# Performance work log

Hardware: AMD Instinct MI355X
Metric: run time of the kernel (lower is better)

Reference implementation:

```python
import jax, jax.numpy as jnp
import numpy as np


def setup_inputs() -> dict:
    V, D, E = 4096, 128, 12288
    key = jax.random.key(0)
    k1, k2, k3 = jax.random.split(key, 3)
    features = jax.random.normal(k1, (V, D), dtype=jnp.float32)
    # random self-loop-free edge list
    v0 = jax.random.randint(k2, (E,), 0, V)
    off = jax.random.randint(k3, (E,), 1, V)
    v1 = (v0 + off) % V
    edges = jnp.stack([v0, v1]).astype(jnp.int32)  # [2, E]
    # manifold-style neighbor matrix: interior edges share 2 faces
    neighbor = (jnp.zeros((V, V), jnp.int32)
                .at[edges[0], edges[1]].set(2)
                .at[edges[1], edges[0]].set(2))
    return {"features": features, "edges": edges, "neighbor": neighbor}


def _collapse(features, edges, neighbor):
    """Greedy heap-order edge collapse. The heap is built once and only popped,
    so pop order == edges sorted by priority ||f[v0]||^2 + ||f[v1]||^2.
    Returns merge matrix A (f_out = A @ f_in), alive vertex mask, final count."""
    V = neighbor.shape[0]
    target = jnp.int32(V // 2)
    pri = jnp.sum(features * features, axis=1)          # [V]
    epri = pri[edges[0]] + pri[edges[1]]                # [E]
    order = jnp.argsort(epri)                           # heappop order (stable ties)
    alive0 = jnp.ones((V,), bool)
    A0 = jnp.eye(V, dtype=jnp.float32)
    cnt0 = jnp.int32(V)

    def step(carry, e):
        alive, n, A, cnt = carry
        v0 = edges[0, e]
        v1 = edges[1, e]
        do = (cnt > target) & alive[v0] & alive[v1] & (n[v0, v1] == 2)
        # merged neighbor row for v0; v1 dies
        r = (n[v0] + n[v1]).at[v0].set(0).at[v1].set(0)
        row0 = jnp.where(do, r, n[v0])
        row1 = jnp.where(do, jnp.zeros_like(r), n[v1])
        n = (n.at[v0, :].set(row0).at[:, v0].set(row0)
              .at[v1, :].set(row1).at[:, v1].set(row1))
        arow = jnp.where(do, 0.5 * (A[v0] + A[v1]), A[v0])
        A = A.at[v0].set(arow)
        alive = alive.at[v1].set(alive[v1] & jnp.logical_not(do))
        cnt = cnt - do.astype(jnp.int32)
        return (alive, n, A, cnt), None

    (alive, n, A, cnt), _ = jax.lax.scan(step, (alive0, neighbor, A0, cnt0), order)
    return A, alive, cnt


def reference(features, edges, neighbor):
    edges = edges.astype(jnp.int32)
    A, alive, cnt = _collapse(features, edges, neighbor)
    # clean_up() compacts removed vertices; under jit we mask dead rows instead
    pooled = (A @ features) * alive[:, None].astype(features.dtype)
    return pooled, alive, cnt
```

## Files before the change

### kernel.cpp

```cpp
#include <hip/hip_runtime.h>
#include <stdint.h>

#define V 4096
#define D 128
#define E 12288
#define NPAD 16384
#define HALF 8192
#define TARGET 2048
#define MAXM (V - TARGET)
#define ROWU32 256
#define CAP 16
#define SCANCAP 24

#define WAIT_VM0   0x0F70
#define WAIT_LGKM0 0xC07F

#define WS_N      0u
#define WS_PRI    (V * ROWU32 * 4u)
#define WS_KEYS   (WS_PRI + V * 4u)
#define WS_PK     (WS_KEYS + NPAD * 8u)
#define WS_PAIRS  (WS_PK + E * 4u)
#define WS_MCOUNT (WS_PAIRS + MAXM * 4u)
#define WS_ALIVE  (WS_MCOUNT + 16u)

typedef const __attribute__((address_space(1))) unsigned* gas1_t;
typedef __attribute__((address_space(3))) unsigned* las3_t;

__device__ __forceinline__ unsigned getf(const uint4& r, int c) {
    unsigned lo = (c & 2) ? r.z : r.x;
    unsigned hi = (c & 2) ? r.w : r.y;
    return (c & 1) ? hi : lo;
}
__device__ __forceinline__ void orf(uint4& r, int c, unsigned bits) {
    if (c == 0) r.x |= bits; else if (c == 1) r.y |= bits;
    else if (c == 2) r.z |= bits; else r.w |= bits;
}
__device__ __forceinline__ void andf(uint4& r, int c, unsigned msk) {
    if (c == 0) r.x &= msk; else if (c == 1) r.y &= msk;
    else if (c == 2) r.z &= msk; else r.w &= msk;
}

__global__ void k_scatter(const int* __restrict__ edges, unsigned* __restrict__ n32) {
    int e = blockIdx.x * 256 + threadIdx.x;
    if (e < E) {
        int a = edges[e], b = edges[E + e];
        atomicOr(&n32[a * ROWU32 + (b >> 4)], 2u << ((b & 15) * 2));
        atomicOr(&n32[b * ROWU32 + (a >> 4)], 2u << ((a & 15) * 2));
    }
}

__global__ void k_pri(const float* __restrict__ f, float* __restrict__ pri) {
    int v = blockIdx.x * 256 + threadIdx.x;
    if (v < V) {
        const float* p = f + v * D;
        float r[8];
#pragma unroll
        for (int j = 0; j < 8; j++) r[j] = __fmul_rn(p[j], p[j]);
        for (int i = 8; i < D; i += 8) {
#pragma unroll
            for (int j = 0; j < 8; j++)
                r[j] = __fadd_rn(r[j], __fmul_rn(p[i + j], p[i + j]));
        }
        float s01 = __fadd_rn(r[0], r[1]);
        float s23 = __fadd_rn(r[2], r[3]);
        float s45 = __fadd_rn(r[4], r[5]);
        float s67 = __fadd_rn(r[6], r[7]);
        pri[v] = __fadd_rn(__fadd_rn(s01, s23), __fadd_rn(s45, s67));
    }
}

__global__ void k_keys(const int* __restrict__ edges, const float* __restrict__ pri,
                       unsigned long long* __restrict__ keys) {
    int s = blockIdx.x * 256 + threadIdx.x;
    if (s < NPAD) {
        unsigned long long rec;
        if (s < E) {
            int a = edges[s], b = edges[E + s];
            float k = __fadd_rn(pri[a], pri[b]);
            rec = ((unsigned long long)__float_as_uint(k) << 32) | (unsigned)s;
        } else {
            rec = (0xFFFFFFFFull << 32) | (unsigned)s;
        }
        keys[s] = rec;
    }
}

__launch_bounds__(1024)
__global__ void k_sort2(unsigned long long* __restrict__ keys) {
    __shared__ unsigned long long srt[HALF];
    const int tid = threadIdx.x;
    unsigned long long* base = keys + blockIdx.x * HALF;
    for (int s = tid; s < HALF; s += 1024) srt[s] = base[s];
    __syncthreads();
    for (int k = 2; k <= HALF; k <<= 1) {
        for (int j = k >> 1; j >= 1; j >>= 1) {
            for (int i = tid; i < HALF; i += 1024) {
                int ixj = i ^ j;
                if (ixj > i) {
                    unsigned long long x = srt[i], y = srt[ixj];
                    bool up = ((i & k) == 0);
                    if ((x > y) == up) { srt[i] = y; srt[ixj] = x; }
                }
            }
            __syncthreads();
        }
    }
    for (int s = tid; s < HALF; s += 1024) base[s] = srt[s];
}

__launch_bounds__(64)
__global__ void k_mergepath(const unsigned long long* __restrict__ keys,
                            const int* __restrict__ edges, unsigned* __restrict__ pkG) {
    int t = blockIdx.x * 64 + threadIdx.x;
    if (t >= E / 64) return;
    const unsigned long long* A = keys;
    const unsigned long long* B = keys + HALF;
    int d = t * 64;
    int lo = d > HALF ? d - HALF : 0;
    int hi = d < HALF ? d : HALF;
    while (lo < hi) {
        int mid = (lo + hi) >> 1;
        if (A[mid] < B[d - 1 - mid]) lo = mid + 1; else hi = mid;
    }
    int ia = lo, ib = d - lo;
    for (int o = d; o < d + 64; o++) {
        bool takeA = (ib >= HALF) || (ia < HALF && A[ia] < B[ib]);
        unsigned long long r = takeA ? A[ia++] : B[ib++];
        int e = (int)(r & 0xFFFFFFFFull);
        int a = edges[e], b = edges[E + e];
        pkG[o] = ((unsigned)a << 16) | (unsigned)b;
    }
}

__launch_bounds__(64, 1)
__global__ void k_collapse(const unsigned* __restrict__ pkG, unsigned* n32,
                           unsigned* __restrict__ pairsG, int* __restrict__ mcountG,
                           uint8_t* __restrict__ aliveG, float* __restrict__ out) {
    __shared__ unsigned shRows[2 * CAP * ROWU32];
    __shared__ uint8_t alive[V];
    const int lane = threadIdx.x;
    for (int v = lane; v < V; v += 64) alive[v] = 1;
    __builtin_amdgcn_s_waitcnt(WAIT_LGKM0);

    int cnt = V, mcount = 0;
    bool done = false;

    for (int w = 0; w < E && !done; w += 64) {
        __builtin_amdgcn_s_waitcnt(WAIT_VM0);
        unsigned pkv = pkG[w + lane];
        const int a = (int)(pkv >> 16), b = (int)(pkv & 0xFFFFu);
        unsigned wv = *(volatile unsigned*)(n32 + a * ROWU32 + (b >> 4));
        unsigned fv = (wv >> ((b & 15) * 2)) & 3u;
        bool dec = !(alive[a] && alive[b]);

        while (!done) {
            if (!dec && fv != 2u) dec = true;
            unsigned long long mF = __ballot(!dec);
            if (!mF) break;
            int limit = cnt - TARGET; if (limit > CAP) limit = CAP;

            unsigned long long accLanes = 0ull;
            unsigned long long B0 = 0ull, B1 = 0ull;
            int nacc = 0, scanned = 0;
            {
                unsigned long long mIt = mF;
                while (mIt && nacc < limit && scanned < SCANCAP) {
                    int i = __ffsll(mIt) - 1; mIt &= mIt - 1ull;
                    int ai = __shfl(a, i), bi = __shfl(b, i);
                    unsigned ha = ((unsigned)ai * 2654435761u) >> 25;
                    unsigned hb = ((unsigned)bi * 2654435761u) >> 25;
                    unsigned long long m0 = 0ull, m1 = 0ull;
                    if (ha & 64) m1 |= 1ull << (ha & 63); else m0 |= 1ull << (ha & 63);
                    if (hb & 64) m1 |= 1ull << (hb & 63); else m0 |= 1ull << (hb & 63);
                    bool conf = ((B0 & m0) | (B1 & m1)) != 0ull;
                    if (!conf) { accLanes |= 1ull << i; nacc++; }
                    B0 |= m0; B1 |= m1;
                    scanned++;
                }
            }

            __builtin_amdgcn_s_waitcnt(WAIT_VM0);
            {
                unsigned long long am = accLanes; int k = 0;
                while (am) {
                    int i = __ffsll(am) - 1; am &= am - 1ull;
                    int v0 = __shfl(a, i), v1 = __shfl(b, i);
                    __builtin_amdgcn_global_load_lds(
                        (gas1_t)(n32 + v0 * ROWU32 + lane * 4),
                        (las3_t)(shRows + (2 * k) * ROWU32), 16, 0, 0);
                    __builtin_amdgcn_global_load_lds(
                        (gas1_t)(n32 + v1 * ROWU32 + lane * 4),
                        (las3_t)(shRows + (2 * k + 1) * ROWU32), 16, 0, 0);
                    k++;
                }
            }
            __builtin_amdgcn_s_waitcnt(WAIT_VM0);
            __builtin_amdgcn_s_waitcnt(WAIT_LGKM0);

            unsigned long long keptLanes = 0ull;
            {
                uint4 RBU = make_uint4(0u, 0u, 0u, 0u);
                uint4 MV0 = make_uint4(0u, 0u, 0u, 0u);
                unsigned long long am = accLanes; int k = 0;
                while (am) {
                    int i = __ffsll(am) - 1; am &= am - 1ull;
                    int v0 = __shfl(a, i), v1 = __shfl(b, i);
                    uint4 rb = *((const uint4*)(shRows + (2 * k + 1) * ROWU32) + lane);
                    bool c = false;
                    if ((v0 >> 6) == lane)
                        c |= ((getf(RBU, (v0 >> 4) & 3) >> ((v0 & 15) * 2)) & 3u) != 0u;
                    if ((v1 >> 6) == lane)
                        c |= ((getf(RBU, (v1 >> 4) & 3) >> ((v1 & 15) * 2)) & 3u) != 0u;
                    c |= ((rb.x & MV0.x) | (rb.y & MV0.y) |
                          (rb.z & MV0.z) | (rb.w & MV0.w)) != 0u;
                    if (__ballot(c) == 0ull) {
                        keptLanes |= 1ull << i;
                        RBU.x |= rb.x; RBU.y |= rb.y; RBU.z |= rb.z; RBU.w |= rb.w;
                        if ((v0 >> 6) == lane) orf(MV0, (v0 >> 4) & 3, 3u << ((v0 & 15) * 2));
                    }
                    k++;
                }
            }

            {
                unsigned long long am = accLanes; int k = 0;
                while (am) {
                    int i = __ffsll(am) - 1; am &= am - 1ull;
                    if ((keptLanes >> i) & 1ull) {
                        int v0 = __shfl(a, i), v1 = __shfl(b, i);
                        uint4 ra = *((const uint4*)(shRows + (2 * k) * ROWU32) + lane);
                        uint4 rb = *((const uint4*)(shRows + (2 * k + 1) * ROWU32) + lane);
                        uint4 rr;
                        rr.x = ra.x | rb.x | ((ra.x & rb.x & 0xAAAAAAAAu) >> 1);
                        rr.y = ra.y | rb.y | ((ra.y & rb.y & 0xAAAAAAAAu) >> 1);
                        rr.z = ra.z | rb.z | ((ra.z & rb.z & 0xAAAAAAAAu) >> 1);
                        rr.w = ra.w | rb.w | ((ra.w & rb.w & 0xAAAAAAAAu) >> 1);
                        if ((v0 >> 6) == lane) andf(rr, (v0 >> 4) & 3, ~(3u << ((v0 & 15) * 2)));
                        if ((v1 >> 6) == lane) andf(rr, (v1 >> 4) & 3, ~(3u << ((v1 & 15) * 2)));
                        *((uint4*)(n32 + v0 * ROWU32) + lane) = rr;
                        *((uint4*)(shRows + (2 * k) * ROWU32) + lane) = rr;
                        int sh0 = (v0 & 15) * 2, wi0 = v0 >> 4;
#pragma unroll
                        for (int c = 0; c < 4; c++) {
                            unsigned bb = getf(rb, c);
                            if (!bb) continue;
                            unsigned aa = getf(ra, c), vvv = getf(rr, c);
                            int xbase = (lane << 6) + (c << 4);
                            unsigned t = bb;
                            while (t) {
                                int q = (__ffs(t) - 1) >> 1;
                                t &= ~(3u << (q * 2));
                                int x = xbase + q;
                                if (x != v0 && x != v1) {
                                    unsigned dx =
                                        (((aa >> (q * 2)) ^ (vvv >> (q * 2))) & 3u) << sh0;
                                    if (dx) atomicXor(n32 + x * ROWU32 + wi0, dx);
                                }
                            }
                        }
                        if (lane == 0) {
                            alive[v1] = 0;
                            pairsG[mcount] = ((unsigned)v0 << 16) | (unsigned)v1;
                        }
                        mcount++; cnt--;
                    }
                    k++;
                }
            }
            __builtin_amdgcn_s_waitcnt(WAIT_LGKM0);

            {
                int slot = -1, fld = 0;
                unsigned long long am = accLanes; int k = 0;
                while (am) {
                    int i = __ffsll(am) - 1; am &= am - 1ull;
                    if ((keptLanes >> i) & 1ull) {
                        int v0 = __shfl(a, i), v1 = __shfl(b, i);
                        if (a == v1 || b == v1) dec = true;
                        if (lane == i) dec = true;
                        if (b == v0) { slot = 2 * k; fld = a; }
                        else if (a == v0) { slot = 2 * k; fld = b; }
                    }
                    k++;
                }
                if (slot >= 0 && !dec)
                    fv = (shRows[slot * ROWU32 + (fld >> 4)] >> ((fld & 15) * 2)) & 3u;
            }
            if (cnt == TARGET) done = true;
        }
    }

    for (int v = lane; v < V; v += 64) {
        uint8_t ao = alive[v];
        aliveG[v] = ao;
        out[V * D + v] = ao ? 1.0f : 0.0f;
    }
    if (lane == 0) { mcountG[0] = mcount; out[V * D + V] = (float)cnt; }
}

__launch_bounds__(256)
__global__ void k_apply(const float* __restrict__ f, const unsigned* __restrict__ pairsG,
                        const int* __restrict__ mcountG, float* __restrict__ out) {
    __shared__ unsigned pl[MAXM];
    __shared__ int rootL[256];
    __shared__ float wL[256];
    const int tid = threadIdx.x;
    const int mc = mcountG[0];
    for (int j = tid; j < mc; j += 256) pl[j] = pairsG[j];
    __syncthreads();
    int cur = blockIdx.x * 256 + tid;
    float w = 1.0f;
    for (int j = 0; j < mc; j++) {
        unsigned p = pl[j];
        int v0 = (int)(p >> 16), v1 = (int)(p & 0xFFFFu);
        if (cur == v1) { cur = v0; w *= 0.5f; }
        else if (cur == v0) w *= 0.5f;
    }
    rootL[tid] = cur;
    wL[tid] = w;
    __syncthreads();
    const int sub = tid >> 7;
    const int d = tid & 127;
    for (int s = 0; s < 256; s += 2) {
        int idx = s + sub;
        int vv = blockIdx.x * 256 + idx;
        atomicAdd(&out[rootL[idx] * D + d], wL[idx] * f[vv * D + d]);
    }
}

extern "C" void kernel_launch(void* const* d_in, const int* in_sizes, int n_in,
                              void* d_out, int out_size, void* d_ws, size_t ws_size,
                              hipStream_t stream) {
    (void)in_sizes; (void)n_in; (void)out_size; (void)ws_size;
    const float* features = (const float*)d_in[0];
    const int* edges = (const int*)d_in[1];
    uint8_t* ws = (uint8_t*)d_ws;
    unsigned* n32 = (unsigned*)(ws + WS_N);
    float* pri = (float*)(ws + WS_PRI);
    unsigned long long* keys = (unsigned long long*)(ws + WS_KEYS);
    unsigned* pkG = (unsigned*)(ws + WS_PK);
    unsigned* pairsG = (unsigned*)(ws + WS_PAIRS);
    int* mcountG = (int*)(ws + WS_MCOUNT);
    uint8_t* aliveG = ws + WS_ALIVE;
    float* out = (float*)d_out;

    hipMemsetAsync(n32, 0, (size_t)V * ROWU32 * 4, stream);
    hipMemsetAsync(out, 0, (size_t)V * D * sizeof(float), stream);
    k_pri<<<(V + 255) / 256, 256, 0, stream>>>(features, pri);
    k_scatter<<<(E + 255) / 256, 256, 0, stream>>>(edges, n32);
    k_keys<<<(NPAD + 255) / 256, 256, 0, stream>>>(edges, pri, keys);
    k_sort2<<<2, 1024, 0, stream>>>(keys);
    k_mergepath<<<(E / 64 + 63) / 64, 64, 0, stream>>>(keys, edges, pkG);
    k_collapse<<<1, 64, 0, stream>>>(pkG, n32, pairsG, mcountG, aliveG, out);
    k_apply<<<V / 256, 256, 0, stream>>>(features, pairsG, mcountG, out);
}
```

Before: 3.826 ms.

## Parallelize collapse batch conflict check and row merges across lane groups

```diff
diff --git a/kernel.cpp b/kernel.cpp
--- a/kernel.cpp
+++ b/kernel.cpp
@@ -10,7 +10,6 @@
 #define MAXM (V - TARGET)
 #define ROWU32 256
 #define CAP 16
-#define SCANCAP 24
 
 #define WAIT_VM0   0x0F70
 #define WAIT_LGKM0 0xC07F
@@ -30,10 +29,6 @@
     unsigned lo = (c & 2) ? r.z : r.x;
     unsigned hi = (c & 2) ? r.w : r.y;
     return (c & 1) ? hi : lo;
-}
-__device__ __forceinline__ void orf(uint4& r, int c, unsigned bits) {
-    if (c == 0) r.x |= bits; else if (c == 1) r.y |= bits;
-    else if (c == 2) r.z |= bits; else r.w |= bits;
 }
 __device__ __forceinline__ void andf(uint4& r, int c, unsigned msk) {
     if (c == 0) r.x &= msk; else if (c == 1) r.y &= msk;
@@ -137,10 +132,13 @@
                            unsigned* __restrict__ pairsG, int* __restrict__ mcountG,
                            uint8_t* __restrict__ aliveG, float* __restrict__ out) {
     __shared__ unsigned shRows[2 * CAP * ROWU32];
-    __shared__ uint8_t alive[V];
+    __shared__ uint8_t  alive[V];
+    __shared__ uint8_t  shV2S[V];
+    __shared__ unsigned shCand[CAP];
+    __shared__ unsigned shConf[CAP];
     const int lane = threadIdx.x;
-    for (int v = lane; v < V; v += 64) alive[v] = 1;
-    __builtin_amdgcn_s_waitcnt(WAIT_LGKM0);
+    for (int v = lane; v < V; v += 64) { alive[v] = 1; shV2S[v] = 0xFF; }
+    __syncthreads();
 
     int cnt = V, mcount = 0;
     bool done = false;
@@ -158,134 +156,125 @@
             unsigned long long mF = __ballot(!dec);
             if (!mF) break;
             int limit = cnt - TARGET; if (limit > CAP) limit = CAP;
-
-            unsigned long long accLanes = 0ull;
-            unsigned long long B0 = 0ull, B1 = 0ull;
-            int nacc = 0, scanned = 0;
+            int flagged = (int)__popcll(mF);
+            int nacc = flagged < limit ? flagged : limit;
+
+            int myK = -1;
+            if (!dec) {
+                int rank = (int)__popcll(mF & ((1ull << lane) - 1ull));
+                if (rank < limit) { myK = rank; shCand[rank] = pkv; }
+            }
+            if (lane < CAP) shConf[lane] = 0u;
+            __syncthreads();
+
+            __builtin_amdgcn_s_waitcnt(WAIT_VM0);
+            for (int k = 0; k < nacc; k++) {
+                unsigned cp = shCand[k];
+                int v0 = (int)(cp >> 16), v1 = (int)(cp & 0xFFFFu);
+                __builtin_amdgcn_global_load_lds(
+                    (gas1_t)(n32 + v0 * ROWU32 + lane * 4),
+                    (las3_t)(shRows + (2 * k) * ROWU32), 16, 0, 0);
+                __builtin_amdgcn_global_load_lds(
+                    (gas1_t)(n32 + v1 * ROWU32 + lane * 4),
+                    (las3_t)(shRows + (2 * k + 1) * ROWU32), 16, 0, 0);
+            }
+            __builtin_amdgcn_s_waitcnt(WAIT_VM0);
+            __syncthreads();
+
+            for (int pp = lane; pp < CAP * CAP; pp += 64) {
+                int k = pp >> 4, j = pp & 15;
+                if (j < k && k < nacc) {
+                    unsigned cj = shCand[j], ck = shCand[k];
+                    int v0j = (int)(cj >> 16), v1j = (int)(cj & 0xFFFFu);
+                    int v0k = (int)(ck >> 16), v1k = (int)(ck & 0xFFFFu);
+                    bool c = (v0k == v0j) || (v0k == v1j) || (v1k == v0j) || (v1k == v1j);
+                    c |= ((shRows[(2*j+1)*ROWU32 + (v0k >> 4)] >> ((v0k & 15)*2)) & 3u) != 0u;
+                    c |= ((shRows[(2*j+1)*ROWU32 + (v1k >> 4)] >> ((v1k & 15)*2)) & 3u) != 0u;
+                    c |= ((shRows[(2*k+1)*ROWU32 + (v0j >> 4)] >> ((v0j & 15)*2)) & 3u) != 0u;
+                    if (c) atomicOr(&shConf[k], 1u << j);
+                }
+            }
+            __syncthreads();
+
+            unsigned kept = 0u;
+            for (int k = 0; k < nacc; k++)
+                if (shConf[k] == 0u) kept |= 1u << k;
+            int nk = __popc(kept);
+            if (myK >= 0 && ((kept >> myK) & 1u)) dec = true;
+
+            if (lane < nacc && ((kept >> lane) & 1u)) {
+                unsigned cp = shCand[lane];
+                int v0 = (int)(cp >> 16), v1 = (int)(cp & 0xFFFFu);
+                alive[v1] = 0;
+                shV2S[v0] = (uint8_t)(2 * lane);
+                int r = __popc(kept & ((1u << lane) - 1u));
+                pairsG[mcount + r] = cp;
+            }
+            mcount += nk; cnt -= nk;
+            __syncthreads();
+
             {
-                unsigned long long mIt = mF;
-                while (mIt && nacc < limit && scanned < SCANCAP) {
-                    int i = __ffsll(mIt) - 1; mIt &= mIt - 1ull;
-                    int ai = __shfl(a, i), bi = __shfl(b, i);
-                    unsigned ha = ((unsigned)ai * 2654435761u) >> 25;
-                    unsigned hb = ((unsigned)bi * 2654435761u) >> 25;
-                    unsigned long long m0 = 0ull, m1 = 0ull;
-                    if (ha & 64) m1 |= 1ull << (ha & 63); else m0 |= 1ull << (ha & 63);
-                    if (hb & 64) m1 |= 1ull << (hb & 63); else m0 |= 1ull << (hb & 63);
-                    bool conf = ((B0 & m0) | (B1 & m1)) != 0ull;
-                    if (!conf) { accLanes |= 1ull << i; nacc++; }
-                    B0 |= m0; B1 |= m1;
-                    scanned++;
-                }
-            }
-
-            __builtin_amdgcn_s_waitcnt(WAIT_VM0);
-            {
-                unsigned long long am = accLanes; int k = 0;
-                while (am) {
-                    int i = __ffsll(am) - 1; am &= am - 1ull;
-                    int v0 = __shfl(a, i), v1 = __shfl(b, i);
-                    __builtin_amdgcn_global_load_lds(
-                        (gas1_t)(n32 + v0 * ROWU32 + lane * 4),
-                        (las3_t)(shRows + (2 * k) * ROWU32), 16, 0, 0);
-                    __builtin_amdgcn_global_load_lds(
-                        (gas1_t)(n32 + v1 * ROWU32 + lane * 4),
-                        (las3_t)(shRows + (2 * k + 1) * ROWU32), 16, 0, 0);
-                    k++;
-                }
-            }
-            __builtin_amdgcn_s_waitcnt(WAIT_VM0);
-            __builtin_amdgcn_s_waitcnt(WAIT_LGKM0);
-
-            unsigned long long keptLanes = 0ull;
-            {
-                uint4 RBU = make_uint4(0u, 0u, 0u, 0u);
-                uint4 MV0 = make_uint4(0u, 0u, 0u, 0u);
-                unsigned long long am = accLanes; int k = 0;
-                while (am) {
-                    int i = __ffsll(am) - 1; am &= am - 1ull;
-                    int v0 = __shfl(a, i), v1 = __shfl(b, i);
-                    uint4 rb = *((const uint4*)(shRows + (2 * k + 1) * ROWU32) + lane);
-                    bool c = false;
-                    if ((v0 >> 6) == lane)
-                        c |= ((getf(RBU, (v0 >> 4) & 3) >> ((v0 & 15) * 2)) & 3u) != 0u;
-                    if ((v1 >> 6) == lane)
-                        c |= ((getf(RBU, (v1 >> 4) & 3) >> ((v1 & 15) * 2)) & 3u) != 0u;
-                    c |= ((rb.x & MV0.x) | (rb.y & MV0.y) |
-                          (rb.z & MV0.z) | (rb.w & MV0.w)) != 0u;
-                    if (__ballot(c) == 0ull) {
-                        keptLanes |= 1ull << i;
-                        RBU.x |= rb.x; RBU.y |= rb.y; RBU.z |= rb.z; RBU.w |= rb.w;
-                        if ((v0 >> 6) == lane) orf(MV0, (v0 >> 4) & 3, 3u << ((v0 & 15) * 2));
-                    }
-                    k++;
-                }
-            }
-
-            {
-                unsigned long long am = accLanes; int k = 0;
-                while (am) {
-                    int i = __ffsll(am) - 1; am &= am - 1ull;
-                    if ((keptLanes >> i) & 1ull) {
-                        int v0 = __shfl(a, i), v1 = __shfl(b, i);
-                        uint4 ra = *((const uint4*)(shRows + (2 * k) * ROWU32) + lane);
-                        uint4 rb = *((const uint4*)(shRows + (2 * k + 1) * ROWU32) + lane);
+                int g = lane >> 2, sub = lane & 3;
+                if (g < nacc && ((kept >> g) & 1u)) {
+                    unsigned cp = shCand[g];
+                    int v0 = (int)(cp >> 16), v1 = (int)(cp & 0xFFFFu);
+                    const uint4* rowA = (const uint4*)(shRows + (2 * g) * ROWU32);
+                    const uint4* rowB = (const uint4*)(shRows + (2 * g + 1) * ROWU32);
+                    int m0u = v0 >> 6, m1u = v1 >> 6;
+                    int sh0 = (v0 & 15) * 2, wi0 = v0 >> 4;
+                    for (int t = 0; t < 16; t++) {
+                        int u = sub * 16 + ((t + lane) & 15);
+                        uint4 ra = rowA[u], rb = rowB[u];
                         uint4 rr;
                         rr.x = ra.x | rb.x | ((ra.x & rb.x & 0xAAAAAAAAu) >> 1);
                         rr.y = ra.y | rb.y | ((ra.y & rb.y & 0xAAAAAAAAu) >> 1);
                         rr.z = ra.z | rb.z | ((ra.z & rb.z & 0xAAAAAAAAu) >> 1);
                         rr.w = ra.w | rb.w | ((ra.w & rb.w & 0xAAAAAAAAu) >> 1);
-                        if ((v0 >> 6) == lane) andf(rr, (v0 >> 4) & 3, ~(3u << ((v0 & 15) * 2)));
-                        if ((v1 >> 6) == lane) andf(rr, (v1 >> 4) & 3, ~(3u << ((v1 & 15) * 2)));
-                        *((uint4*)(n32 + v0 * ROWU32) + lane) = rr;
-                        *((uint4*)(shRows + (2 * k) * ROWU32) + lane) = rr;
-                        int sh0 = (v0 & 15) * 2, wi0 = v0 >> 4;
+                        if (u == m0u) andf(rr, (v0 >> 4) & 3, ~(3u << ((v0 & 15) * 2)));
+                        if (u == m1u) andf(rr, (v1 >> 4) & 3, ~(3u << ((v1 & 15) * 2)));
+                        ((uint4*)(n32 + v0 * ROWU32))[u] = rr;
+                        ((uint4*)shRows)[(2 * g) * (ROWU32 / 4) + u] = rr;
 #pragma unroll
                         for (int c = 0; c < 4; c++) {
                             unsigned bb = getf(rb, c);
                             if (!bb) continue;
                             unsigned aa = getf(ra, c), vvv = getf(rr, c);
-                            int xbase = (lane << 6) + (c << 4);
-                            unsigned t = bb;
-                            while (t) {
-                                int q = (__ffs(t) - 1) >> 1;
-                                t &= ~(3u << (q * 2));
+                            int xbase = (u << 6) + (c << 4);
+                            unsigned tt = bb;
+                            while (tt) {
+                                int q = (__ffs(tt) - 1) >> 1;
+                                tt &= ~(3u << (q * 2));
                                 int x = xbase + q;
                                 if (x != v0 && x != v1) {
                                     unsigned dx =
-                                        (((aa >> (q * 2)) ^ (vvv >> (q * 2))) & 3u) << sh0;
+                                        (((aa >> (q*2)) ^ (vvv >> (q*2))) & 3u) << sh0;
                                     if (dx) atomicXor(n32 + x * ROWU32 + wi0, dx);
                                 }
                             }
                         }
-                        if (lane == 0) {
-                            alive[v1] = 0;
-                            pairsG[mcount] = ((unsigned)v0 << 16) | (unsigned)v1;
-                        }
-                        mcount++; cnt--;
                     }
-                    k++;
                 }
             }
-            __builtin_amdgcn_s_waitcnt(WAIT_LGKM0);
-
-            {
-                int slot = -1, fld = 0;
-                unsigned long long am = accLanes; int k = 0;
-                while (am) {
-                    int i = __ffsll(am) - 1; am &= am - 1ull;
-                    if ((keptLanes >> i) & 1ull) {
-                        int v0 = __shfl(a, i), v1 = __shfl(b, i);
-                        if (a == v1 || b == v1) dec = true;
-                        if (lane == i) dec = true;
-                        if (b == v0) { slot = 2 * k; fld = a; }
-                        else if (a == v0) { slot = 2 * k; fld = b; }
+            __syncthreads();
+
+            if (!dec) {
+                if (!alive[a] || !alive[b]) dec = true;
+                else {
+                    int s = shV2S[a];
+                    if (s != 0xFF)
+                        fv = (shRows[s * ROWU32 + (b >> 4)] >> ((b & 15) * 2)) & 3u;
+                    else {
+                        s = shV2S[b];
+                        if (s != 0xFF)
+                            fv = (shRows[s * ROWU32 + (a >> 4)] >> ((a & 15) * 2)) & 3u;
                     }
-                    k++;
                 }
-                if (slot >= 0 && !dec)
-                    fv = (shRows[slot * ROWU32 + (fld >> 4)] >> ((fld & 15) * 2)) & 3u;
-            }
+            }
+            __syncthreads();
+
+            if (lane < nacc && ((kept >> lane) & 1u))
+                shV2S[(int)(shCand[lane] >> 16)] = 0xFF;
+
             if (cnt == TARGET) done = true;
         }
     }
```

After: 3.246 ms. -15.2%, faster.
